# Kernel tuning notes

Hardware: AMD Instinct MI355X
Metric: run time of the kernel (lower is better)

## Reference

```python
import jax, jax.numpy as jnp
import numpy as np

N_NODES = 50000
NUM_HEAD = 2
NEG_SLOPE_ATT = 0.2
NEG_SLOPE_ACT = 0.3


def _glorot(key, shape):
    fan = shape[-1] + (shape[-2] if len(shape) > 1 else shape[-1])
    lim = jnp.sqrt(6.0 / fan)
    return jax.random.uniform(key, shape, jnp.float32, -lim, lim)


def gat_conv(h, src, dst, W, att, bias):
    # h: (N, in_dim); W: (out_dim, in_dim) torch Linear layout; att: (1, H, 2k)
    N = h.shape[0]
    H = att.shape[1]
    k = att.shape[2] // 2
    x = (h @ W.T).reshape(N, H, k)
    x_i = x[dst]  # target features (E, H, k)
    x_j = x[src]  # source features (E, H, k)
    # alpha = sum(cat([x_i, x_j]) * att) without materializing the concat
    alpha = jnp.einsum('ehk,hk->eh', x_i, att[0, :, :k]) + jnp.einsum('ehk,hk->eh', x_j, att[0, :, k:])
    alpha = jax.nn.leaky_relu(alpha, NEG_SLOPE_ATT)
    # segment softmax grouped by edge_index[0] (src), as in the original code
    m = jax.ops.segment_max(alpha, src, num_segments=N)
    e = jnp.exp(alpha - m[src])
    s = jax.ops.segment_sum(e, src, num_segments=N)
    alpha = e / (s[src] + 1e-16)
    msg = x_j * alpha[:, :, None]
    out = jax.ops.segment_sum(msg, dst, num_segments=N)  # aggregate to targets
    out = out.reshape(N, H * k) + bias
    return jax.nn.relu(out)


def _forward(x, src, dst, node_index, params):
    (W1, att1, b1, W2, att2, b2, W3, att3, b3, W_out, b_out) = params
    h = gat_conv(x, src, dst, W1, att1, b1)
    h = jax.nn.leaky_relu(h, NEG_SLOPE_ACT)
    h = gat_conv(h, src, dst, W2, att2, b2)
    h = jax.nn.leaky_relu(h, NEG_SLOPE_ACT)
    h = gat_conv(h, src, dst, W3, att3, b3)
    x_embed = jax.nn.leaky_relu(h, NEG_SLOPE_ACT)
    output = x_embed @ W_out.T + b_out
    node_output = output[node_index]
    ypred = jnp.argmax(output, axis=1)
    y_nodepred = ypred[node_index]
    return x_embed, node_output, ypred, y_nodepred


def setup_inputs() -> dict:
    key = jax.random.key(0)
    ks = jax.random.split(key, 16)
    N, E, D = N_NODES, 800000, 128
    H, k = NUM_HEAD, 128 // NUM_HEAD
    inp = {
        'x': jax.random.normal(ks[0], (N, D), jnp.float32),
        'edge_index': jax.random.randint(ks[1], (2, E), 0, N, jnp.int64),
        'node_label': jax.random.normal(ks[2], (1000, 1, 3), jnp.float32),
        'node_index': jax.random.randint(ks[3], (1000,), 0, N, jnp.int64),
        'W1': _glorot(ks[4], (D, D)),
        'att1': _glorot(ks[5], (1, H, 2 * k)),
        'b1': jnp.zeros((D,), jnp.float32),
        'W2': _glorot(ks[6], (D, D)),
        'att2': _glorot(ks[7], (1, H, 2 * k)),
        'b2': jnp.zeros((D,), jnp.float32),
        'W3': _glorot(ks[8], (D, D)),
        'att3': _glorot(ks[9], (1, H, 2 * k)),
        'b3': jnp.zeros((D,), jnp.float32),
        'W_out': _glorot(ks[10], (3, D)),
        'b_out': jnp.zeros((3,), jnp.float32),
    }
    return inp


def reference(x, edge_index, node_label, node_index, W1, att1, b1, W2, att2, b2, W3, att3, b3, W_out, b_out):
    N = x.shape[0]
    loop = jnp.arange(N, dtype=edge_index.dtype)
    src = jnp.concatenate([edge_index[0], loop])  # add_self_loops
    dst = jnp.concatenate([edge_index[1], loop])
    params = (W1, att1, b1, W2, att2, b2, W3, att3, b3, W_out, b_out)
    return _forward(x, src, dst, node_index, params)
```

## Files before the change

kernel.cpp:

```cpp
#include <hip/hip_runtime.h>
#include <math.h>


#define EPB 4096

__global__ __launch_bounds__(256) void gemm128(const float* __restrict__ A,
                                               const float* __restrict__ Wm,
                                               const float* __restrict__ att,
                                               float* __restrict__ C,
                                               float4* __restrict__ ni4,
                                               float2* __restrict__ ad2v, int N) {
    __shared__ float As[64][68];
    __shared__ float Wt[64][132];
    const int tx = threadIdx.x;
    const int row0 = blockIdx.x * 64;
    const int cid = tx & 31;
    const int rid = tx >> 5;
    float acc[8][4] = {};
    const float4* A4 = (const float4*)A;
    const float4* W4 = (const float4*)Wm;

    for (int kt = 0; kt < 2; ++kt) {
        for (int i = tx; i < 1024; i += 256) {
            int r = i >> 4, q = i & 15;
            int row = row0 + r;
            float4 v = (row < N) ? A4[(size_t)row * 32 + kt * 16 + q]
                                 : make_float4(0.f, 0.f, 0.f, 0.f);
            As[r][q * 4 + 0] = v.x; As[r][q * 4 + 1] = v.y;
            As[r][q * 4 + 2] = v.z; As[r][q * 4 + 3] = v.w;
        }
        for (int i = tx; i < 2048; i += 256) {
            int c = i >> 4, q = i & 15;
            float4 v = W4[(size_t)c * 32 + kt * 16 + q];
            Wt[q * 4 + 0][c] = v.x; Wt[q * 4 + 1][c] = v.y;
            Wt[q * 4 + 2][c] = v.z; Wt[q * 4 + 3][c] = v.w;
        }
        __syncthreads();
        for (int k = 0; k < 64; k += 4) {
            float4 a[8];
            #pragma unroll
            for (int i = 0; i < 8; ++i) a[i] = *(const float4*)&As[rid * 8 + i][k];
            #pragma unroll
            for (int kk = 0; kk < 4; ++kk) {
                float4 w = *(const float4*)&Wt[k + kk][cid * 4];
                #pragma unroll
                for (int i = 0; i < 8; ++i) {
                    float av = (kk == 0) ? a[i].x : (kk == 1) ? a[i].y : (kk == 2) ? a[i].z : a[i].w;
                    acc[i][0] += av * w.x; acc[i][1] += av * w.y;
                    acc[i][2] += av * w.z; acc[i][3] += av * w.w;
                }
            }
        }
        __syncthreads();
    }
    #pragma unroll
    for (int i = 0; i < 8; ++i) {
        int row = row0 + rid * 8 + i;
        if (row < N)
            ((float4*)C)[(size_t)row * 32 + cid] =
                make_float4(acc[i][0], acc[i][1], acc[i][2], acc[i][3]);
    }
    const int hh = cid >> 4;
    const int c0 = (cid & 15) * 4;
    float ad0 = att[hh * 128 + c0 + 0], ad1 = att[hh * 128 + c0 + 1];
    float ad2c = att[hh * 128 + c0 + 2], ad3 = att[hh * 128 + c0 + 3];
    float as0 = att[hh * 128 + 64 + c0 + 0], as1 = att[hh * 128 + 64 + c0 + 1];
    float as2 = att[hh * 128 + 64 + c0 + 2], as3 = att[hh * 128 + 64 + c0 + 3];
    float pd[8], ps[8];
    #pragma unroll
    for (int i = 0; i < 8; ++i) {
        pd[i] = acc[i][0] * ad0 + acc[i][1] * ad1 + acc[i][2] * ad2c + acc[i][3] * ad3;
        ps[i] = acc[i][0] * as0 + acc[i][1] * as1 + acc[i][2] * as2 + acc[i][3] * as3;
    }
    #pragma unroll
    for (int m = 1; m < 16; m <<= 1) {
        #pragma unroll
        for (int i = 0; i < 8; ++i) {
            pd[i] += __shfl_xor(pd[i], m);
            ps[i] += __shfl_xor(ps[i], m);
        }
    }
    const int ll = tx & 63;
    const int grp = ll & 32;
    #pragma unroll
    for (int i = 0; i < 8; ++i) {
        float d0 = __shfl(pd[i], grp + 0);
        float d1 = __shfl(pd[i], grp + 16);
        float s0 = __shfl(ps[i], grp + 0);
        float s1 = __shfl(ps[i], grp + 16);
        if ((ll & 31) == 0) {
            int row = row0 + rid * 8 + i;
            if (row < N) {
                ad2v[row] = make_float2(d0, d1);
                ni4[row] = make_float4(s0, s1, 0.f, 0.f);
            }
        }
    }
}

__global__ __launch_bounds__(256) void hist_both(const int* __restrict__ ei, int E,
                                                 unsigned int* __restrict__ dd,
                                                 unsigned int* __restrict__ ds) {
    int e = blockIdx.x * 256 + threadIdx.x;
    if (e < E) {
        atomicAdd(&ds[ei[e]], 1u);
        atomicAdd(&dd[ei[E + e]], 1u);
    }
}

__global__ __launch_bounds__(256) void scan_p1(const unsigned int* __restrict__ deg_d,
                                               const unsigned int* __restrict__ deg_s,
                                               unsigned int* __restrict__ off_dv,
                                               unsigned int* __restrict__ off_sv,
                                               unsigned int* __restrict__ bsum_dv,
                                               unsigned int* __restrict__ bsum_sv,
                                               int N, int NB) {
    __shared__ unsigned int sh[256];
    const bool isS = (int)blockIdx.x >= NB;
    const unsigned int* deg = isS ? deg_s : deg_d;
    unsigned int* off  = isS ? off_sv  : off_dv;
    unsigned int* bsum = isS ? bsum_sv : bsum_dv;
    const int blk = isS ? (blockIdx.x - NB) : blockIdx.x;
    int t = threadIdx.x;
    int base = blk * 1024 + t * 4;
    unsigned int v0 = 0, v1 = 0, v2 = 0, v3 = 0;
    if (base + 3 < N) {
        uint4 q = *(const uint4*)&deg[base];
        v0 = q.x + 1u; v1 = q.y + 1u; v2 = q.z + 1u; v3 = q.w + 1u;
    } else {
        if (base + 0 < N) v0 = deg[base + 0] + 1u;
        if (base + 1 < N) v1 = deg[base + 1] + 1u;
        if (base + 2 < N) v2 = deg[base + 2] + 1u;
        if (base + 3 < N) v3 = deg[base + 3] + 1u;
    }
    sh[t] = v0 + v1 + v2 + v3;
    __syncthreads();
    #pragma unroll
    for (int d = 1; d < 256; d <<= 1) {
        unsigned int u = (t >= d) ? sh[t - d] : 0u;
        __syncthreads();
        sh[t] += u;
        __syncthreads();
    }
    unsigned int ex = (t == 0) ? 0u : sh[t - 1];
    if (base + 3 < N) {
        *(uint4*)&off[base] = make_uint4(ex, ex + v0, ex + v0 + v1, ex + v0 + v1 + v2);
    } else {
        if (base + 0 < N) off[base + 0] = ex;
        if (base + 1 < N) off[base + 1] = ex + v0;
        if (base + 2 < N) off[base + 2] = ex + v0 + v1;
        if (base + 3 < N) off[base + 3] = ex + v0 + v1 + v2;
    }
    if (t == 255) bsum[blk] = sh[255];
}

__global__ __launch_bounds__(1024) void scan_p2(unsigned int* __restrict__ bsum_d,
                                                unsigned int* __restrict__ bsum_s, int NB) {
    __shared__ unsigned int sh[1024];
    unsigned int* bsum = blockIdx.x ? bsum_s : bsum_d;
    int t = threadIdx.x;
    sh[t] = (t < NB) ? bsum[t] : 0u;
    __syncthreads();
    #pragma unroll
    for (int d = 1; d < 1024; d <<= 1) {
        unsigned int u = (t >= d) ? sh[t - d] : 0u;
        __syncthreads();
        sh[t] += u;
        __syncthreads();
    }
    if (t < NB) bsum[t] = (t == 0) ? 0u : sh[t - 1];
}

__global__ __launch_bounds__(256) void scan_p3(unsigned int* __restrict__ off_dv,
                                               unsigned int* __restrict__ off_sv,
                                               const unsigned int* __restrict__ bsum_dv,
                                               const unsigned int* __restrict__ bsum_sv,
                                               unsigned int* __restrict__ cur_dv,
                                               unsigned int* __restrict__ cur_sv,
                                               int N, unsigned int total, int half) {
    const bool isS = (int)blockIdx.x >= half;
    unsigned int* off = isS ? off_sv : off_dv;
    const unsigned int* bsum = isS ? bsum_sv : bsum_dv;
    unsigned int* cur = isS ? cur_sv : cur_dv;
    const int blk = isS ? (blockIdx.x - half) : blockIdx.x;
    int i = blk * 256 + threadIdx.x;
    if (i < N) {
        unsigned int v = off[i] + bsum[i >> 10];
        off[i] = v;
        if ((i & 63) == 0) cur[i >> 6] = v;
    }
    if (i == N) off[N] = total;
}

template <bool BYDST>
__global__ __launch_bounds__(512) void coarse_scatter(const int* __restrict__ ei, int E, int Et,
                                                      unsigned int* __restrict__ cur,
                                                      unsigned int* __restrict__ tmp, int CB) {
    __shared__ unsigned int lh[800];
    const int t = threadIdx.x;
    for (int b = t; b < CB; b += 512) lh[b] = 0u;
    __syncthreads();
    const int i0 = blockIdx.x * EPB;
    for (int i = t; i < EPB; i += 512) {
        int e = i0 + i;
        if (e < Et) {
            int k = (e < E) ? ei[BYDST ? (E + e) : e] : (e - E);
            atomicAdd(&lh[k >> 6], 1u);
        }
    }
    __syncthreads();
    for (int b = t; b < CB; b += 512) {
        unsigned int c = lh[b];
        lh[b] = atomicAdd(&cur[b], c);
    }
    __syncthreads();
    for (int i = t; i < EPB; i += 512) {
        int e = i0 + i;
        if (e < Et) {
            int s, d;
            if (e < E) { s = ei[e]; d = ei[E + e]; } else { s = d = e - E; }
            int k = BYDST ? d : s;
            int v = BYDST ? s : d;
            unsigned int pos = atomicAdd(&lh[k >> 6], 1u);
            tmp[pos] = ((unsigned int)(k & 63) << 16) | (unsigned int)v;
        }
    }
}

__global__ __launch_bounds__(256) void fine_sort(const unsigned int* __restrict__ tmp,
                                                 const unsigned int* __restrict__ off,
                                                 int* __restrict__ outv, int N) {
    __shared__ unsigned int h[64];
    const int b = blockIdx.x;
    const int node0 = b * 64;
    int nn = N - node0; if (nn > 64) nn = 64;
    const int t = threadIdx.x;
    if (t < nn) h[t] = off[node0 + t];
    __syncthreads();
    unsigned int base = off[node0];
    unsigned int end = off[node0 + nn];
    for (unsigned int i = base + t; i < end; i += 256) {
        unsigned int v = tmp[i];
        unsigned int pos = atomicAdd(&h[v >> 16], 1u);
        outv[pos] = (int)(v & 0xFFFFu);
    }
}

__global__ __launch_bounds__(256) void src_sum(const int* __restrict__ dsts,
                                               const unsigned int* __restrict__ off_s,
                                               const float2* __restrict__ ad2,
                                               float* __restrict__ ni, int N) {
    int n = blockIdx.x * 256 + threadIdx.x;
    if (n >= N) return;
    float as0 = ni[(size_t)n * 4 + 0];
    float as1 = ni[(size_t)n * 4 + 1];
    unsigned int j0 = off_s[n], j1 = off_s[n + 1];
    float s0 = 0.f, s1 = 0.f;
    unsigned int j = j0;
    for (; j + 4 <= j1; j += 4) {
        int d0 = dsts[j], d1 = dsts[j + 1], d2 = dsts[j + 2], d3 = dsts[j + 3];
        float2 a0 = ad2[d0], a1 = ad2[d1], a2 = ad2[d2], a3 = ad2[d3];
        float t;
        t = as0 + a0.x; t = (t > 0.f) ? t : 0.2f * t; s0 += __expf(t);
        t = as1 + a0.y; t = (t > 0.f) ? t : 0.2f * t; s1 += __expf(t);
        t = as0 + a1.x; t = (t > 0.f) ? t : 0.2f * t; s0 += __expf(t);
        t = as1 + a1.y; t = (t > 0.f) ? t : 0.2f * t; s1 += __expf(t);
        t = as0 + a2.x; t = (t > 0.f) ? t : 0.2f * t; s0 += __expf(t);
        t = as1 + a2.y; t = (t > 0.f) ? t : 0.2f * t; s1 += __expf(t);
        t = as0 + a3.x; t = (t > 0.f) ? t : 0.2f * t; s0 += __expf(t);
        t = as1 + a3.y; t = (t > 0.f) ? t : 0.2f * t; s1 += __expf(t);
    }
    for (; j < j1; ++j) {
        float2 a = ad2[dsts[j]];
        float t;
        t = as0 + a.x; t = (t > 0.f) ? t : 0.2f * t; s0 += __expf(t);
        t = as1 + a.y; t = (t > 0.f) ? t : 0.2f * t; s1 += __expf(t);
    }
    ni[(size_t)n * 4 + 2] = 1.0f / (s0 + 1e-16f);
    ni[(size_t)n * 4 + 3] = 1.0f / (s1 + 1e-16f);
}

__global__ __launch_bounds__(256) void edge_w(const int* __restrict__ srcs,
                                              const unsigned int* __restrict__ off_d,
                                              const float4* __restrict__ ni4,
                                              const float2* __restrict__ ad2,
                                              float2* __restrict__ w2, int N) {
    __shared__ unsigned int lb[65];
    __shared__ float2 lad[64];
    const int node0 = blockIdx.x * 64;
    int nn = N - node0; if (nn > 64) nn = 64;
    const int t = threadIdx.x;
    if (t <= nn) lb[t] = off_d[node0 + t];
    if (t < nn) lad[t] = ad2[node0 + t];
    __syncthreads();
    unsigned int base = lb[0], end = lb[nn];
    for (unsigned int i = base + t; i < end; i += 256) {
        int lo = 0, hi = nn;
        while (hi - lo > 1) {
            int mid = (lo + hi) >> 1;
            if (i >= lb[mid]) lo = mid; else hi = mid;
        }
        float2 ad = lad[lo];
        int s = srcs[i];
        float4 nv = ni4[s];
        float a0 = ad.x + nv.x; a0 = (a0 > 0.f) ? a0 : 0.2f * a0;
        float a1 = ad.y + nv.y; a1 = (a1 > 0.f) ? a1 : 0.2f * a1;
        w2[i] = make_float2(__expf(a0) * nv.z, __expf(a1) * nv.w);
    }
}

template <int U>
__device__ __forceinline__ void agg_edges(unsigned int j, const int* __restrict__ srcs,
                                          const float2* __restrict__ w2,
                                          const float2* __restrict__ x2,
                                          int l, int hi, float& accx, float& accy) {
    int s[U]; float2 w[U]; float2 v[U];
    #pragma unroll
    for (int u = 0; u < U; ++u) s[u] = srcs[j + u];
    #pragma unroll
    for (int u = 0; u < U; ++u) w[u] = w2[j + u];
    #pragma unroll
    for (int u = 0; u < U; ++u) v[u] = x2[(size_t)s[u] * 64 + l];
    #pragma unroll
    for (int u = 0; u < U; ++u) {
        float ww = hi ? w[u].y : w[u].x;
        accx += v[u].x * ww;
        accy += v[u].y * ww;
    }
}

template <bool LAST>
__global__ __launch_bounds__(256) void agg_csr(const int* __restrict__ srcs,
                                               const unsigned int* __restrict__ off,
                                               const float2* __restrict__ x2,
                                               const float2* __restrict__ w2,
                                               const float* __restrict__ bias,
                                               float* __restrict__ out,
                                               const float* __restrict__ Wout,
                                               const float* __restrict__ bout,
                                               float* __restrict__ out3,
                                               float* __restrict__ ypred, int N) {
    int d = blockIdx.x * 4 + (threadIdx.x >> 6);
    int l = threadIdx.x & 63;
    if (d >= N) return;
    d = __builtin_amdgcn_readfirstlane(d);
    const int hi = l >> 5;
    unsigned int j0 = off[d], j1 = off[d + 1];
    float accx = 0.f, accy = 0.f;
    unsigned int j = j0;
    for (; j + 16 <= j1; j += 16) agg_edges<16>(j, srcs, w2, x2, l, hi, accx, accy);
    if (j + 8 <= j1) { agg_edges<8>(j, srcs, w2, x2, l, hi, accx, accy); j += 8; }
    if (j + 4 <= j1) { agg_edges<4>(j, srcs, w2, x2, l, hi, accx, accy); j += 4; }
    if (j + 2 <= j1) { agg_edges<2>(j, srcs, w2, x2, l, hi, accx, accy); j += 2; }
    if (j < j1)      { agg_edges<1>(j, srcs, w2, x2, l, hi, accx, accy); }

    float2 bb = ((const float2*)bias)[l];
    float o0 = fmaxf(accx + bb.x, 0.f);
    float o1 = fmaxf(accy + bb.y, 0.f);
    ((float2*)out)[(size_t)d * 64 + l] = make_float2(o0, o1);
    if (LAST) {
        const float2* W2 = (const float2*)Wout;
        float2 wa = W2[l], wb = W2[64 + l], wc = W2[128 + l];
        float p0 = o0 * wa.x + o1 * wa.y;
        float p1 = o0 * wb.x + o1 * wb.y;
        float p2 = o0 * wc.x + o1 * wc.y;
        #pragma unroll
        for (int m = 32; m; m >>= 1) {
            p0 += __shfl_xor(p0, m);
            p1 += __shfl_xor(p1, m);
            p2 += __shfl_xor(p2, m);
        }
        if (l == 0) {
            p0 += bout[0]; p1 += bout[1]; p2 += bout[2];
            out3[d * 3 + 0] = p0; out3[d * 3 + 1] = p1; out3[d * 3 + 2] = p2;
            int am = 0; float best = p0;
            if (p1 > best) { best = p1; am = 1; }
            if (p2 > best) { best = p2; am = 2; }
            ypred[d] = (float)am;
        }
    }
}

__global__ __launch_bounds__(256) void gather_out(const float* __restrict__ out3,
                                                  const float* __restrict__ ypred,
                                                  const int* __restrict__ node_index,
                                                  float* __restrict__ node_out,
                                                  float* __restrict__ y_nodepred, int M) {
    int i = blockIdx.x * 256 + threadIdx.x;
    if (i >= M) return;
    int idx = node_index[i];
    node_out[i * 3 + 0] = out3[idx * 3 + 0];
    node_out[i * 3 + 1] = out3[idx * 3 + 1];
    node_out[i * 3 + 2] = out3[idx * 3 + 2];
    y_nodepred[i] = ypred[idx];
}

extern "C" void kernel_launch(void* const* d_in, const int* in_sizes, int n_in,
                              void* d_out, int out_size, void* d_ws, size_t ws_size,
                              hipStream_t stream) {
    const float* x          = (const float*)d_in[0];
    const int*   ei         = (const int*)d_in[1];
    const int*   node_index = (const int*)d_in[3];
    const float* W[3]   = {(const float*)d_in[4], (const float*)d_in[7], (const float*)d_in[10]};
    const float* att[3] = {(const float*)d_in[5], (const float*)d_in[8], (const float*)d_in[11]};
    const float* b[3]   = {(const float*)d_in[6], (const float*)d_in[9], (const float*)d_in[12]};
    const float* Wout = (const float*)d_in[13];
    const float* bout = (const float*)d_in[14];

    const int N  = in_sizes[0] / 128;
    const int E  = in_sizes[1] / 2;
    const int Et = E + N;
    const int M  = in_sizes[3];
    const int NB = (N + 1023) / 1024;
    const int CB = (N + 63) / 64;
    const int NBLK = (Et + EPB - 1) / EPB;

    float* ws     = (float*)d_ws;
    float* xlin   = ws;
    unsigned int* tmp = (unsigned int*)ws;
    float* hb     = xlin + (size_t)N * 128;
    float* ad     = hb + (size_t)N * 128;
    float* ni     = ad + (size_t)N * 2;
    float* out3   = ad;
    unsigned int* off_d = (unsigned int*)(ni + (size_t)N * 4);
    unsigned int* off_s = off_d + (size_t)N + 4;
    unsigned int* deg_d = off_s + (size_t)N + 4;
    unsigned int* deg_s = deg_d + (size_t)N;
    unsigned int* cur_d = deg_s + (size_t)N;
    unsigned int* cur_s = cur_d + 1024;
    unsigned int* bsum_d = cur_s + 1024;
    unsigned int* bsum_s = bsum_d + 1024;
    int* srcs = (int*)(bsum_s + 1024);
    int* dsts = srcs + (size_t)Et;
    float2* w2 = (float2*)(dsts + (size_t)Et);

    float* o_embed = (float*)d_out;
    float* o_node  = o_embed + (size_t)N * 128;
    float* o_ypred = o_node + (size_t)M * 3;
    float* o_ynode = o_ypred + (size_t)N;

    const int gemm_blocks = (N + 63) / 64;
    const int node_wave_blocks = (N + 3) / 4;
    const int n_blocks = (N + 255) / 256;
    const int p3_half = (N + 256) / 256;

    hipMemsetAsync(deg_d, 0, (size_t)2 * N * sizeof(unsigned int), stream);
    hist_both<<<(E + 255) / 256, 256, 0, stream>>>(ei, E, deg_d, deg_s);
    scan_p1<<<2 * NB, 256, 0, stream>>>(deg_d, deg_s, off_d, off_s, bsum_d, bsum_s, N, NB);
    scan_p2<<<2, 1024, 0, stream>>>(bsum_d, bsum_s, NB);
    scan_p3<<<2 * p3_half, 256, 0, stream>>>(off_d, off_s, bsum_d, bsum_s, cur_d, cur_s,
                                             N, (unsigned int)Et, p3_half);
    coarse_scatter<true><<<NBLK, 512, 0, stream>>>(ei, E, Et, cur_d, tmp, CB);
    fine_sort<<<CB, 256, 0, stream>>>(tmp, off_d, srcs, N);
    coarse_scatter<false><<<NBLK, 512, 0, stream>>>(ei, E, Et, cur_s, tmp, CB);
    fine_sort<<<CB, 256, 0, stream>>>(tmp, off_s, dsts, N);

    for (int L = 0; L < 3; ++L) {
        const float* hin = (L == 0) ? x : hb;
        gemm128<<<gemm_blocks, 256, 0, stream>>>(hin, W[L], att[L], xlin,
                                                 (float4*)ni, (float2*)ad, N);
        src_sum<<<n_blocks, 256, 0, stream>>>(dsts, off_s, (const float2*)ad, ni, N);
        edge_w<<<CB, 256, 0, stream>>>(srcs, off_d, (const float4*)ni, (const float2*)ad,
                                       w2, N);
        if (L < 2)
            agg_csr<false><<<node_wave_blocks, 256, 0, stream>>>(
                srcs, off_d, (const float2*)xlin, (const float2*)w2,
                b[L], hb, nullptr, nullptr, nullptr, nullptr, N);
        else
            agg_csr<true><<<node_wave_blocks, 256, 0, stream>>>(
                srcs, off_d, (const float2*)xlin, (const float2*)w2,
                b[L], o_embed, Wout, bout, out3, o_ypred, N);
    }
    gather_out<<<(M + 255) / 256, 256, 0, stream>>>(out3, o_ypred, node_index, o_node, o_ynode, M);
}
```

Before: 471.7 us.

## Replace per-node degree histogram and scan with coarse bucket sort for both CSRs

Drops the per-node degree histogram with global atomics and the three-pass scan over N nodes. It now builds a shared-memory histogram over coarse 64-node buckets, scans those buckets in a single block, and lets fine_sort derive the per-node offsets locally. The dst and src sorts are fused into single scatter and fine-sort launches with separate tmp buffers, and EPB is doubled. The aim is fewer launches and fewer global atomics in graph preprocessing, at the cost of a second tmp buffer and of reading the edge list twice in the combined kernels.

```diff
diff --git a/kernel.cpp b/kernel.cpp
--- a/kernel.cpp
+++ b/kernel.cpp
@@ -2,7 +2,7 @@
 #include <math.h>
 
 
-#define EPB 4096
+#define EPB 8192
 
 __global__ __launch_bounds__(256) void gemm128(const float* __restrict__ A,
                                                const float* __restrict__ Wm,
@@ -98,148 +98,145 @@
     }
 }
 
-__global__ __launch_bounds__(256) void hist_both(const int* __restrict__ ei, int E,
-                                                 unsigned int* __restrict__ dd,
-                                                 unsigned int* __restrict__ ds) {
-    int e = blockIdx.x * 256 + threadIdx.x;
-    if (e < E) {
-        atomicAdd(&ds[ei[e]], 1u);
-        atomicAdd(&dd[ei[E + e]], 1u);
-    }
-}
-
-__global__ __launch_bounds__(256) void scan_p1(const unsigned int* __restrict__ deg_d,
-                                               const unsigned int* __restrict__ deg_s,
-                                               unsigned int* __restrict__ off_dv,
-                                               unsigned int* __restrict__ off_sv,
-                                               unsigned int* __restrict__ bsum_dv,
-                                               unsigned int* __restrict__ bsum_sv,
-                                               int N, int NB) {
-    __shared__ unsigned int sh[256];
-    const bool isS = (int)blockIdx.x >= NB;
-    const unsigned int* deg = isS ? deg_s : deg_d;
-    unsigned int* off  = isS ? off_sv  : off_dv;
-    unsigned int* bsum = isS ? bsum_sv : bsum_dv;
-    const int blk = isS ? (blockIdx.x - NB) : blockIdx.x;
-    int t = threadIdx.x;
-    int base = blk * 1024 + t * 4;
-    unsigned int v0 = 0, v1 = 0, v2 = 0, v3 = 0;
-    if (base + 3 < N) {
-        uint4 q = *(const uint4*)&deg[base];
-        v0 = q.x + 1u; v1 = q.y + 1u; v2 = q.z + 1u; v3 = q.w + 1u;
-    } else {
-        if (base + 0 < N) v0 = deg[base + 0] + 1u;
-        if (base + 1 < N) v1 = deg[base + 1] + 1u;
-        if (base + 2 < N) v2 = deg[base + 2] + 1u;
-        if (base + 3 < N) v3 = deg[base + 3] + 1u;
-    }
-    sh[t] = v0 + v1 + v2 + v3;
-    __syncthreads();
-    #pragma unroll
-    for (int d = 1; d < 256; d <<= 1) {
-        unsigned int u = (t >= d) ? sh[t - d] : 0u;
-        __syncthreads();
-        sh[t] += u;
-        __syncthreads();
-    }
-    unsigned int ex = (t == 0) ? 0u : sh[t - 1];
-    if (base + 3 < N) {
-        *(uint4*)&off[base] = make_uint4(ex, ex + v0, ex + v0 + v1, ex + v0 + v1 + v2);
-    } else {
-        if (base + 0 < N) off[base + 0] = ex;
-        if (base + 1 < N) off[base + 1] = ex + v0;
-        if (base + 2 < N) off[base + 2] = ex + v0 + v1;
-        if (base + 3 < N) off[base + 3] = ex + v0 + v1 + v2;
-    }
-    if (t == 255) bsum[blk] = sh[255];
-}
-
-__global__ __launch_bounds__(1024) void scan_p2(unsigned int* __restrict__ bsum_d,
-                                                unsigned int* __restrict__ bsum_s, int NB) {
-    __shared__ unsigned int sh[1024];
-    unsigned int* bsum = blockIdx.x ? bsum_s : bsum_d;
-    int t = threadIdx.x;
-    sh[t] = (t < NB) ? bsum[t] : 0u;
-    __syncthreads();
-    #pragma unroll
-    for (int d = 1; d < 1024; d <<= 1) {
-        unsigned int u = (t >= d) ? sh[t - d] : 0u;
-        __syncthreads();
-        sh[t] += u;
-        __syncthreads();
-    }
-    if (t < NB) bsum[t] = (t == 0) ? 0u : sh[t - 1];
-}
-
-__global__ __launch_bounds__(256) void scan_p3(unsigned int* __restrict__ off_dv,
-                                               unsigned int* __restrict__ off_sv,
-                                               const unsigned int* __restrict__ bsum_dv,
-                                               const unsigned int* __restrict__ bsum_sv,
-                                               unsigned int* __restrict__ cur_dv,
-                                               unsigned int* __restrict__ cur_sv,
-                                               int N, unsigned int total, int half) {
-    const bool isS = (int)blockIdx.x >= half;
-    unsigned int* off = isS ? off_sv : off_dv;
-    const unsigned int* bsum = isS ? bsum_sv : bsum_dv;
-    unsigned int* cur = isS ? cur_sv : cur_dv;
-    const int blk = isS ? (blockIdx.x - half) : blockIdx.x;
-    int i = blk * 256 + threadIdx.x;
-    if (i < N) {
-        unsigned int v = off[i] + bsum[i >> 10];
-        off[i] = v;
-        if ((i & 63) == 0) cur[i >> 6] = v;
-    }
-    if (i == N) off[N] = total;
-}
-
-template <bool BYDST>
-__global__ __launch_bounds__(512) void coarse_scatter(const int* __restrict__ ei, int E, int Et,
-                                                      unsigned int* __restrict__ cur,
-                                                      unsigned int* __restrict__ tmp, int CB) {
-    __shared__ unsigned int lh[800];
+__global__ __launch_bounds__(512) void coarse_hist(const int* __restrict__ ei, int E, int Et,
+                                                   unsigned int* __restrict__ gh_d,
+                                                   unsigned int* __restrict__ gh_s, int CB) {
+    __shared__ unsigned int lh_d[800];
+    __shared__ unsigned int lh_s[800];
     const int t = threadIdx.x;
-    for (int b = t; b < CB; b += 512) lh[b] = 0u;
+    for (int b = t; b < CB; b += 512) { lh_d[b] = 0u; lh_s[b] = 0u; }
     __syncthreads();
     const int i0 = blockIdx.x * EPB;
-    for (int i = t; i < EPB; i += 512) {
-        int e = i0 + i;
-        if (e < Et) {
-            int k = (e < E) ? ei[BYDST ? (E + e) : e] : (e - E);
-            atomicAdd(&lh[k >> 6], 1u);
-        }
-    }
-    __syncthreads();
-    for (int b = t; b < CB; b += 512) {
-        unsigned int c = lh[b];
-        lh[b] = atomicAdd(&cur[b], c);
-    }
-    __syncthreads();
     for (int i = t; i < EPB; i += 512) {
         int e = i0 + i;
         if (e < Et) {
             int s, d;
             if (e < E) { s = ei[e]; d = ei[E + e]; } else { s = d = e - E; }
-            int k = BYDST ? d : s;
-            int v = BYDST ? s : d;
-            unsigned int pos = atomicAdd(&lh[k >> 6], 1u);
-            tmp[pos] = ((unsigned int)(k & 63) << 16) | (unsigned int)v;
-        }
-    }
-}
-
-__global__ __launch_bounds__(256) void fine_sort(const unsigned int* __restrict__ tmp,
-                                                 const unsigned int* __restrict__ off,
-                                                 int* __restrict__ outv, int N) {
+            atomicAdd(&lh_d[d >> 6], 1u);
+            atomicAdd(&lh_s[s >> 6], 1u);
+        }
+    }
+    __syncthreads();
+    for (int b = t; b < CB; b += 512) {
+        if (lh_d[b]) atomicAdd(&gh_d[b], lh_d[b]);
+        if (lh_s[b]) atomicAdd(&gh_s[b], lh_s[b]);
+    }
+}
+
+__global__ __launch_bounds__(1024) void coarse_scan(const unsigned int* __restrict__ gh_d,
+                                                    const unsigned int* __restrict__ gh_s,
+                                                    unsigned int* __restrict__ coff_d,
+                                                    unsigned int* __restrict__ coff_s,
+                                                    unsigned int* __restrict__ cur_d,
+                                                    unsigned int* __restrict__ cur_s,
+                                                    int CB, unsigned int total) {
+    __shared__ unsigned int sh[1024];
+    const int t = threadIdx.x;
+    for (int a = 0; a < 2; ++a) {
+        const unsigned int* gh = a ? gh_s : gh_d;
+        unsigned int* coff = a ? coff_s : coff_d;
+        unsigned int* cur  = a ? cur_s : cur_d;
+        sh[t] = (t < CB) ? gh[t] : 0u;
+        __syncthreads();
+        #pragma unroll
+        for (int d = 1; d < 1024; d <<= 1) {
+            unsigned int u = (t >= d) ? sh[t - d] : 0u;
+            __syncthreads();
+            sh[t] += u;
+            __syncthreads();
+        }
+        if (t < CB) {
+            unsigned int ex = (t == 0) ? 0u : sh[t - 1];
+            coff[t] = ex;
+            cur[t] = ex;
+        }
+        if (t == 0) coff[CB] = total;
+        __syncthreads();
+    }
+}
+
+__global__ __launch_bounds__(512) void coarse_scatter_both(const int* __restrict__ ei,
+                                                           int E, int Et,
+                                                           unsigned int* __restrict__ cur_d,
+                                                           unsigned int* __restrict__ cur_s,
+                                                           unsigned int* __restrict__ tmp_d,
+                                                           unsigned int* __restrict__ tmp_s,
+                                                           int CB) {
+    __shared__ unsigned int lh_d[800];
+    __shared__ unsigned int lh_s[800];
+    const int t = threadIdx.x;
+    for (int b = t; b < CB; b += 512) { lh_d[b] = 0u; lh_s[b] = 0u; }
+    __syncthreads();
+    const int i0 = blockIdx.x * EPB;
+    for (int i = t; i < EPB; i += 512) {
+        int e = i0 + i;
+        if (e < Et) {
+            int s, d;
+            if (e < E) { s = ei[e]; d = ei[E + e]; } else { s = d = e - E; }
+            atomicAdd(&lh_d[d >> 6], 1u);
+            atomicAdd(&lh_s[s >> 6], 1u);
+        }
+    }
+    __syncthreads();
+    for (int b = t; b < CB; b += 512) {
+        unsigned int cd = lh_d[b], cs = lh_s[b];
+        lh_d[b] = cd ? atomicAdd(&cur_d[b], cd) : 0u;
+        lh_s[b] = cs ? atomicAdd(&cur_s[b], cs) : 0u;
+    }
+    __syncthreads();
+    for (int i = t; i < EPB; i += 512) {
+        int e = i0 + i;
+        if (e < Et) {
+            int s, d;
+            if (e < E) { s = ei[e]; d = ei[E + e]; } else { s = d = e - E; }
+            unsigned int pd = atomicAdd(&lh_d[d >> 6], 1u);
+            tmp_d[pd] = ((unsigned int)(d & 63) << 16) | (unsigned int)s;
+            unsigned int ps = atomicAdd(&lh_s[s >> 6], 1u);
+            tmp_s[ps] = ((unsigned int)(s & 63) << 16) | (unsigned int)d;
+        }
+    }
+}
+
+__global__ __launch_bounds__(256) void fine_sort(const unsigned int* __restrict__ tmp_d,
+                                                 const unsigned int* __restrict__ tmp_s,
+                                                 const unsigned int* __restrict__ coff_d,
+                                                 const unsigned int* __restrict__ coff_s,
+                                                 unsigned int* __restrict__ off_d,
+                                                 unsigned int* __restrict__ off_s,
+                                                 int* __restrict__ srcs,
+                                                 int* __restrict__ dsts,
+                                                 int N, int CB, unsigned int total) {
+    __shared__ unsigned int cnt[64];
     __shared__ unsigned int h[64];
-    const int b = blockIdx.x;
+    const bool isS = (int)blockIdx.x >= CB;
+    const int b = isS ? (blockIdx.x - CB) : blockIdx.x;
+    const unsigned int* tmp  = isS ? tmp_s : tmp_d;
+    const unsigned int* coff = isS ? coff_s : coff_d;
+    unsigned int* off = isS ? off_s : off_d;
+    int* outv = isS ? dsts : srcs;
     const int node0 = b * 64;
     int nn = N - node0; if (nn > 64) nn = 64;
     const int t = threadIdx.x;
-    if (t < nn) h[t] = off[node0 + t];
-    __syncthreads();
-    unsigned int base = off[node0];
-    unsigned int end = off[node0 + nn];
-    for (unsigned int i = base + t; i < end; i += 256) {
+    const unsigned int cb0 = coff[b], cb1 = coff[b + 1];
+    if (t < 64) cnt[t] = 0u;
+    __syncthreads();
+    for (unsigned int i = cb0 + t; i < cb1; i += 256)
+        atomicAdd(&cnt[tmp[i] >> 16], 1u);
+    __syncthreads();
+    if (t < 64) h[t] = cnt[t];
+    __syncthreads();
+    #pragma unroll
+    for (int d = 1; d < 64; d <<= 1) {
+        unsigned int u = (t < 64 && t >= d) ? h[t - d] : 0u;
+        __syncthreads();
+        if (t < 64) h[t] += u;
+        __syncthreads();
+    }
+    if (t < 64) h[t] = cb0 + h[t] - cnt[t];
+    __syncthreads();
+    if (t < nn) off[node0 + t] = h[t];
+    if (b == CB - 1 && t == 0) off[N] = total;
+    for (unsigned int i = cb0 + t; i < cb1; i += 256) {
         unsigned int v = tmp[i];
         unsigned int pos = atomicAdd(&h[v >> 16], 1u);
         outv[pos] = (int)(v & 0xFFFFu);
@@ -411,26 +408,26 @@
     const int E  = in_sizes[1] / 2;
     const int Et = E + N;
     const int M  = in_sizes[3];
-    const int NB = (N + 1023) / 1024;
     const int CB = (N + 63) / 64;
     const int NBLK = (Et + EPB - 1) / EPB;
 
     float* ws     = (float*)d_ws;
     float* xlin   = ws;
-    unsigned int* tmp = (unsigned int*)ws;
+    unsigned int* tmp_d = (unsigned int*)ws;
+    unsigned int* tmp_s = tmp_d + (size_t)Et;
     float* hb     = xlin + (size_t)N * 128;
     float* ad     = hb + (size_t)N * 128;
     float* ni     = ad + (size_t)N * 2;
     float* out3   = ad;
     unsigned int* off_d = (unsigned int*)(ni + (size_t)N * 4);
     unsigned int* off_s = off_d + (size_t)N + 4;
-    unsigned int* deg_d = off_s + (size_t)N + 4;
-    unsigned int* deg_s = deg_d + (size_t)N;
-    unsigned int* cur_d = deg_s + (size_t)N;
-    unsigned int* cur_s = cur_d + 1024;
-    unsigned int* bsum_d = cur_s + 1024;
-    unsigned int* bsum_s = bsum_d + 1024;
-    int* srcs = (int*)(bsum_s + 1024);
+    unsigned int* gh_d  = off_s + (size_t)N + 4;
+    unsigned int* gh_s  = gh_d + 1024;
+    unsigned int* coff_d = gh_s + 1024;
+    unsigned int* coff_s = coff_d + 1024;
+    unsigned int* cur_d  = coff_s + 1024;
+    unsigned int* cur_s  = cur_d + 1024;
+    int* srcs = (int*)(cur_s + 1024);
     int* dsts = srcs + (size_t)Et;
     float2* w2 = (float2*)(dsts + (size_t)Et);
 
@@ -442,18 +439,14 @@
     const int gemm_blocks = (N + 63) / 64;
     const int node_wave_blocks = (N + 3) / 4;
     const int n_blocks = (N + 255) / 256;
-    const int p3_half = (N + 256) / 256;
-
-    hipMemsetAsync(deg_d, 0, (size_t)2 * N * sizeof(unsigned int), stream);
-    hist_both<<<(E + 255) / 256, 256, 0, stream>>>(ei, E, deg_d, deg_s);
-    scan_p1<<<2 * NB, 256, 0, stream>>>(deg_d, deg_s, off_d, off_s, bsum_d, bsum_s, N, NB);
-    scan_p2<<<2, 1024, 0, stream>>>(bsum_d, bsum_s, NB);
-    scan_p3<<<2 * p3_half, 256, 0, stream>>>(off_d, off_s, bsum_d, bsum_s, cur_d, cur_s,
-                                             N, (unsigned int)Et, p3_half);
-    coarse_scatter<true><<<NBLK, 512, 0, stream>>>(ei, E, Et, cur_d, tmp, CB);
-    fine_sort<<<CB, 256, 0, stream>>>(tmp, off_d, srcs, N);
-    coarse_scatter<false><<<NBLK, 512, 0, stream>>>(ei, E, Et, cur_s, tmp, CB);
-    fine_sort<<<CB, 256, 0, stream>>>(tmp, off_s, dsts, N);
+
+    hipMemsetAsync(gh_d, 0, 2048 * sizeof(unsigned int), stream);
+    coarse_hist<<<NBLK, 512, 0, stream>>>(ei, E, Et, gh_d, gh_s, CB);
+    coarse_scan<<<1, 1024, 0, stream>>>(gh_d, gh_s, coff_d, coff_s, cur_d, cur_s,
+                                        CB, (unsigned int)Et);
+    coarse_scatter_both<<<NBLK, 512, 0, stream>>>(ei, E, Et, cur_d, cur_s, tmp_d, tmp_s, CB);
+    fine_sort<<<2 * CB, 256, 0, stream>>>(tmp_d, tmp_s, coff_d, coff_s, off_d, off_s,
+                                          srcs, dsts, N, CB, (unsigned int)Et);
 
     for (int L = 0; L < 3; ++L) {
         const float* hin = (L == 0) ? x : hb;
```

Result: faster. 419.3 us (-11.1%).
